# Kernel tuning notes

Measured on AMD Instinct MI355X. Metric: run time of the kernel, lower is better.

## Reference

```python
import jax, jax.numpy as jnp
import numpy as np

CLASS_TOKEN_INDEX = 1
MAX_PROMPTS = 25
MAX_TEXT_LEN = 3500
THRESHOLD = 0.5
B, S, D, E = 8, 4096, 768, 128
P = E * (E - 1) // 2  # 8128 candidate span pairs


def setup_inputs() -> dict:
    rng = np.random.default_rng(0)
    input_ids = rng.integers(5, 30000, size=(B, S)).astype(np.int64)
    words_mask = np.zeros((B, S), dtype=np.int64)
    attention_mask = np.zeros((B, S), dtype=np.int64)
    text_lengths = np.zeros((B, 1), dtype=np.int64)
    for b in range(B):
        ns = int(rng.integers(10, MAX_PROMPTS + 1))  # number of entity-type prompt tokens
        input_ids[b][input_ids[b] == CLASS_TOKEN_INDEX] = 5  # remove stray specials
        input_ids[b, :ns] = CLASS_TOKEN_INDEX
        L = int(rng.integers(3000, MAX_TEXT_LEN + 1))  # number of words in text
        words_mask[b, ns:ns + L] = np.arange(1, L + 1)
        attention_mask[b, :ns + L] = 1
        text_lengths[b, 0] = L
    key = jax.random.key(0)
    k1, k2, k3 = jax.random.split(key, 3)
    return {
        "token_embeds": jax.random.normal(k1, (B, S, D), dtype=jnp.float32),
        "adj": jax.random.uniform(k2, (B, E, E), dtype=jnp.float32),
        "span_rep": jax.random.normal(k3, (B, E, D), dtype=jnp.float32),
        "input_ids": jnp.asarray(input_ids),
        "attention_mask": jnp.asarray(attention_mask),
        "text_lengths": jnp.asarray(text_lengths),
        "words_mask": jnp.asarray(words_mask),
    }


def _extract_special(token_embeds, input_ids):
    # pack embeddings at positions where input_ids == class token, left-aligned
    special = input_ids == CLASS_TOKEN_INDEX                      # (B,S)
    num_special = special.sum(-1, keepdims=True)                  # (B,1)
    slot = jnp.cumsum(special, axis=-1) - 1                       # packed slot per special
    tgt = jnp.where(special, slot, MAX_PROMPTS)                   # dump pads into extra slot
    bidx = jnp.arange(B)[:, None]
    emb = jnp.zeros((B, MAX_PROMPTS + 1, D), token_embeds.dtype)
    emb = emb.at[bidx, tgt].add(token_embeds * special[..., None].astype(token_embeds.dtype))
    emb = emb[:, :MAX_PROMPTS]
    mask = (jnp.arange(MAX_PROMPTS)[None, :] < num_special).astype(jnp.int64)
    return emb, mask


def _extract_words(token_embeds, words_mask, text_lengths):
    # scatter token embeddings into word slots: words_embedding[b, words_mask[b,j]-1] = token_embeds[b,j]
    is_word = words_mask > 0
    tgt = jnp.where(is_word, words_mask - 1, MAX_TEXT_LEN)        # dump pads into extra slot
    bidx = jnp.arange(B)[:, None]
    we = jnp.zeros((B, MAX_TEXT_LEN + 1, D), token_embeds.dtype)
    we = we.at[bidx, tgt].add(token_embeds * is_word[..., None].astype(token_embeds.dtype))
    we = we[:, :MAX_TEXT_LEN]
    mask = jnp.arange(MAX_TEXT_LEN)[None, :] < text_lengths       # (B,MAX_TEXT_LEN) bool
    return we, mask


def _build_entity_pairs(adj, span_rep):
    rows, cols = jnp.triu_indices(E, k=1)                         # (P,), (P,)
    vals = adj[:, rows, cols]                                     # (B,P)
    sel = vals > THRESHOLD
    # stable left-packing: selected pairs first, preserving triu order (matches per-batch torch loop)
    order = jnp.argsort((~sel).astype(jnp.int32), axis=1, stable=True)
    pair_mask = jnp.take_along_axis(sel, order, axis=1)           # (B,P) bool
    r = rows[order]                                               # (B,P)
    c = cols[order]
    pair_idx = jnp.where(pair_mask[..., None], jnp.stack([r, c], axis=-1), -1)
    bidx = jnp.arange(B)[:, None]
    head_rep = span_rep[bidx, jnp.where(pair_mask, r, 0)]         # pads gather span 0 (clamp_min(0))
    tail_rep = span_rep[bidx, jnp.where(pair_mask, c, 0)]
    return pair_idx, pair_mask, head_rep, tail_rep


def reference(token_embeds, adj, span_rep, input_ids, attention_mask, text_lengths, words_mask):
    prompts_embedding, prompts_embedding_mask = _extract_special(token_embeds, input_ids)
    words_embedding, word_mask = _extract_words(token_embeds, words_mask, text_lengths)
    pair_idx, pair_mask, head_rep, tail_rep = _build_entity_pairs(adj, span_rep)
    return (prompts_embedding, prompts_embedding_mask, words_embedding, word_mask,
            pair_idx, pair_mask, head_rep, tail_rep)
```

## Files before the change

### kernel.cpp

```cpp
#include <hip/hip_runtime.h>

#define BB 8
#define SS 4096
#define DD 768
#define EE 128
#define PP 8128
#define MP 25
#define MT 3500
#define D4 192
#define NROWS_W  (BB*MT)
#define NROWS_P  (BB*PP)
#define NROWS_PR (BB*MP)
#define R_TOTAL  (NROWS_W + 2*NROWS_P + NROWS_PR)

typedef float f32x4 __attribute__((ext_vector_type(4)));

__global__ __launch_bounds__(1024) void k_prep(
    const int* __restrict__ ids, const float* __restrict__ adj,
    const int* __restrict__ wm, const int* __restrict__ tlen,
    float* __restrict__ out3,
    int* __restrict__ wordpos, int* __restrict__ pairrec,
    int* __restrict__ pos, int* __restrict__ nspec)
{
    int b = blockIdx.x;
    int t = threadIdx.x, wave = t >> 6, lane = t & 63;
    __shared__ int pos_s[MP];
    __shared__ int spos[16 * 32];
    __shared__ int wcnt[16];
    __shared__ int woff[17];
    __shared__ int wsum[16];

    if (t < MP) pos_s[t] = -1;

    {
        const int* row = ids + b * SS;
        int base = 0;
        for (int c = 0; c < 4; ++c) {
            int p = wave * 256 + c * 64 + lane;
            bool s = (row[p] == 1);
            unsigned long long m = __ballot(s);
            if (s) {
                int sl = base + __popcll(m & ((1ull << lane) - 1ull));
                if (sl < 32) spos[wave * 32 + sl] = p;
            }
            base += __popcll(m);
        }
        if (lane == 0) wcnt[wave] = base;
    }
    __syncthreads();
    if (t == 0) {
        int acc = 0;
        for (int w = 0; w < 16; ++w) { woff[w] = acc; acc += wcnt[w]; }
        woff[16] = acc;
    }
    __syncthreads();
    {
        int cnt = wcnt[wave]; if (cnt > 32) cnt = 32;
        if (lane < cnt) {
            int g = woff[wave] + lane;
            if (g < MP) pos_s[g] = spos[wave * 32 + lane];
        }
    }

    int L = tlen[b];
    for (int i = t; i < MT; i += 1024) {
        out3[b * MT + i] = (i < L) ? 1.0f : 0.0f;
        wordpos[b * MT + i] = -1;
    }
    __syncthreads();

    for (int i = t; i < SS; i += 1024) {
        int v = wm[b * SS + i];
        if (v > 0 && v <= MT) wordpos[b * MT + v - 1] = i;
    }
    if (t < MP) pos[b * MP + t] = pos_s[t];
    if (t == 0) nspec[b] = woff[16];

    int r8[8], c8[8]; bool s8[8]; int my = 0;
    for (int i = 0; i < 8; ++i) {
        int p = t * 8 + i;
        r8[i] = 0; c8[i] = 0; s8[i] = false;
        if (p < PP) {
            int lo = 0, hi = EE - 2;
            while (lo < hi) {
                int mid = (lo + hi + 1) >> 1;
                int st = mid * (2 * EE - 1 - mid) / 2;
                if (st <= p) lo = mid; else hi = mid - 1;
            }
            int r = lo;
            int st = r * (2 * EE - 1 - r) / 2;
            int c = r + 1 + (p - st);
            r8[i] = r; c8[i] = c;
            s8[i] = adj[((size_t)b * EE + r) * EE + c] > 0.5f;
            my += s8[i] ? 1 : 0;
        }
    }
    int inc = my;
    for (int off = 1; off < 64; off <<= 1) {
        int n = __shfl_up(inc, off);
        if (lane >= off) inc += n;
    }
    if (lane == 63) wsum[wave] = inc;
    __syncthreads();
    int wv_off = 0, K = 0;
    for (int w = 0; w < 16; ++w) {
        int s = wsum[w];
        if (w < wave) wv_off += s;
        K += s;
    }
    int selb = wv_off + inc - my;
    for (int i = 0; i < 8; ++i) {
        int p = t * 8 + i;
        if (p >= PP) break;
        int q;
        if (s8[i]) { q = selb; ++selb; }
        else       { q = K + (p - selb); }
        unsigned rec = s8[i] ? (0x80000000u | ((unsigned)r8[i] << 8) | (unsigned)c8[i]) : 0u;
        pairrec[(size_t)b * PP + q] = (int)rec;
    }
}

__global__ __launch_bounds__(256) void k_gather(
    const float* __restrict__ te, const float* __restrict__ sr,
    const int* __restrict__ wordpos, const int* __restrict__ pairrec,
    const int* __restrict__ pos, const int* __restrict__ nspec,
    float* __restrict__ out0, float* __restrict__ out1, float* __restrict__ out2,
    float* __restrict__ out4, float* __restrict__ out5,
    float* __restrict__ out6, float* __restrict__ out7)
{
    int gw = blockIdx.x * 4 + (threadIdx.x >> 6);
    int lane = threadIdx.x & 63;
    int nw = gridDim.x * 4;
    const f32x4* te4 = (const f32x4*)te;
    const f32x4* sr4 = (const f32x4*)sr;
    for (int row = gw; row < R_TOTAL; row += nw) {
        const f32x4* src4;
        f32x4* dst4;
        bool valid = true;
        bool stream_src = false;
        if (row < NROWS_W) {
            int b = row / MT;
            int s = wordpos[row];
            valid = (s >= 0);
            src4 = te4 + ((size_t)(b * SS + s)) * D4;
            dst4 = (f32x4*)out2 + (size_t)row * D4;
            stream_src = true;
        } else if (row < NROWS_W + 2 * NROWS_P) {
            int idx2 = row - NROWS_W;
            bool head = idx2 < NROWS_P;
            int idx = head ? idx2 : idx2 - NROWS_P;
            int b = idx / PP;
            unsigned rec = (unsigned)pairrec[idx];
            int r = (rec >> 8) & 0x7F;
            int c = rec & 0xFF;
            int s = head ? r : c;
            src4 = sr4 + ((size_t)(b * EE + s)) * D4;
            dst4 = (f32x4*)(head ? out6 : out7) + (size_t)idx * D4;
            if (head && lane == 0) {
                bool sel = rec != 0u;
                out4[(size_t)idx * 2 + 0] = sel ? (float)r : -1.0f;
                out4[(size_t)idx * 2 + 1] = sel ? (float)c : -1.0f;
                out5[idx] = sel ? 1.0f : 0.0f;
            }
        } else {
            int j2 = row - (NROWS_W + 2 * NROWS_P);
            int b = j2 / MP;
            int j = j2 - b * MP;
            int s = pos[j2];
            valid = (s >= 0);
            src4 = te4 + ((size_t)(b * SS + s)) * D4;
            dst4 = (f32x4*)out0 + (size_t)j2 * D4;
            stream_src = true;
            if (lane == 0) out1[j2] = (j < nspec[b]) ? 1.0f : 0.0f;
        }
        #pragma unroll
        for (int k = 0; k < 3; ++k) {
            f32x4 v = (f32x4)(0.0f);
            if (valid) {
                v = stream_src ? __builtin_nontemporal_load(&src4[lane + 64 * k])
                               : src4[lane + 64 * k];
            }
            dst4[lane + 64 * k] = v;
        }
    }
}

extern "C" void kernel_launch(void* const* d_in, const int* in_sizes, int n_in,
                              void* d_out, int out_size, void* d_ws, size_t ws_size,
                              hipStream_t stream) {
    const float* te   = (const float*)d_in[0];
    const float* adj  = (const float*)d_in[1];
    const float* sr   = (const float*)d_in[2];
    const int*   ids  = (const int*)d_in[3];
    const int*   tlen = (const int*)d_in[5];
    const int*   wm   = (const int*)d_in[6];
    float* out = (float*)d_out;

    size_t off0 = 0;
    size_t off1 = off0 + (size_t)BB * MP * DD;
    size_t off2 = off1 + (size_t)BB * MP;
    size_t off3 = off2 + (size_t)BB * MT * DD;
    size_t off4 = off3 + (size_t)BB * MT;
    size_t off5 = off4 + (size_t)BB * PP * 2;
    size_t off6 = off5 + (size_t)BB * PP;
    size_t off7 = off6 + (size_t)BB * PP * DD;

    int* wordpos = (int*)d_ws;
    int* pairrec = wordpos + BB * MT;
    int* pos     = pairrec + BB * PP;
    int* nspec   = pos + BB * MP;

    k_prep<<<BB, 1024, 0, stream>>>(ids, adj, wm, tlen, out + off3,
                                    wordpos, pairrec, pos, nspec);
    k_gather<<<2048, 256, 0, stream>>>(te, sr, wordpos, pairrec, pos, nspec,
                                       out + off0, out + off1, out + off2,
                                       out + off4, out + off5,
                                       out + off6, out + off7);
}
```

Before: 150.4 us.

## Split prep kernel into role blocks and prefetch next row index in gather

```diff
diff --git a/kernel.cpp b/kernel.cpp
--- a/kernel.cpp
+++ b/kernel.cpp
@@ -15,28 +15,29 @@
 
 typedef float f32x4 __attribute__((ext_vector_type(4)));
 
-__global__ __launch_bounds__(1024) void k_prep(
+__global__ __launch_bounds__(256) void k_prep(
     const int* __restrict__ ids, const float* __restrict__ adj,
     const int* __restrict__ wm, const int* __restrict__ tlen,
-    float* __restrict__ out3,
+    float* __restrict__ out1, float* __restrict__ out3,
+    float* __restrict__ out4, float* __restrict__ out5,
     int* __restrict__ wordpos, int* __restrict__ pairrec,
-    int* __restrict__ pos, int* __restrict__ nspec)
+    int* __restrict__ pos)
 {
-    int b = blockIdx.x;
+    int blk = blockIdx.x;
+    int role = blk >> 3, b = blk & 7;
     int t = threadIdx.x, wave = t >> 6, lane = t & 63;
-    __shared__ int pos_s[MP];
-    __shared__ int spos[16 * 32];
-    __shared__ int wcnt[16];
-    __shared__ int woff[17];
-    __shared__ int wsum[16];
-
-    if (t < MP) pos_s[t] = -1;
-
-    {
+
+    if (role == 0) {
+        __shared__ int pos_s[32];
+        __shared__ int spos[4 * 32];
+        __shared__ int wcnt[4];
+        __shared__ int woff[5];
+        if (t < 32) pos_s[t] = -1;
+        __syncthreads();
         const int* row = ids + b * SS;
         int base = 0;
-        for (int c = 0; c < 4; ++c) {
-            int p = wave * 256 + c * 64 + lane;
+        for (int c = 0; c < 16; ++c) {
+            int p = wave * 1024 + c * 64 + lane;
             bool s = (row[p] == 1);
             unsigned long long m = __ballot(s);
             if (s) {
@@ -46,86 +47,117 @@
             base += __popcll(m);
         }
         if (lane == 0) wcnt[wave] = base;
-    }
-    __syncthreads();
-    if (t == 0) {
-        int acc = 0;
-        for (int w = 0; w < 16; ++w) { woff[w] = acc; acc += wcnt[w]; }
-        woff[16] = acc;
-    }
-    __syncthreads();
-    {
-        int cnt = wcnt[wave]; if (cnt > 32) cnt = 32;
-        if (lane < cnt) {
-            int g = woff[wave] + lane;
-            if (g < MP) pos_s[g] = spos[wave * 32 + lane];
-        }
-    }
-
-    int L = tlen[b];
-    for (int i = t; i < MT; i += 1024) {
-        out3[b * MT + i] = (i < L) ? 1.0f : 0.0f;
-        wordpos[b * MT + i] = -1;
-    }
-    __syncthreads();
-
-    for (int i = t; i < SS; i += 1024) {
-        int v = wm[b * SS + i];
-        if (v > 0 && v <= MT) wordpos[b * MT + v - 1] = i;
-    }
-    if (t < MP) pos[b * MP + t] = pos_s[t];
-    if (t == 0) nspec[b] = woff[16];
-
-    int r8[8], c8[8]; bool s8[8]; int my = 0;
-    for (int i = 0; i < 8; ++i) {
-        int p = t * 8 + i;
-        r8[i] = 0; c8[i] = 0; s8[i] = false;
-        if (p < PP) {
+        __syncthreads();
+        if (t == 0) {
+            int acc = 0;
+            for (int w = 0; w < 4; ++w) { woff[w] = acc; acc += wcnt[w]; }
+            woff[4] = acc;
+        }
+        __syncthreads();
+        {
+            int cnt = wcnt[wave]; if (cnt > 32) cnt = 32;
+            if (lane < cnt) {
+                int g = woff[wave] + lane;
+                if (g < MP) pos_s[g] = spos[wave * 32 + lane];
+            }
+        }
+        __syncthreads();
+        if (t < MP) {
+            pos[b * MP + t] = pos_s[t];
+            out1[b * MP + t] = (t < woff[4]) ? 1.0f : 0.0f;
+        }
+    } else if (role == 1) {
+        int L = tlen[b];
+        for (int i = t; i < MT; i += 256) {
+            out3[b * MT + i] = (i < L) ? 1.0f : 0.0f;
+            wordpos[b * MT + i] = -1;
+        }
+        __syncthreads();
+        #pragma unroll 4
+        for (int i = t; i < SS; i += 256) {
+            int v = wm[b * SS + i];
+            if (v > 0 && v <= MT) wordpos[b * MT + v - 1] = i;
+        }
+    } else {
+        __shared__ int wsum[4];
+        int p0 = t * 32;
+        bool act = p0 < PP;
+        int r0 = 0, c0 = 0;
+        if (act) {
             int lo = 0, hi = EE - 2;
             while (lo < hi) {
                 int mid = (lo + hi + 1) >> 1;
                 int st = mid * (2 * EE - 1 - mid) / 2;
-                if (st <= p) lo = mid; else hi = mid - 1;
-            }
-            int r = lo;
-            int st = r * (2 * EE - 1 - r) / 2;
-            int c = r + 1 + (p - st);
-            r8[i] = r; c8[i] = c;
-            s8[i] = adj[((size_t)b * EE + r) * EE + c] > 0.5f;
-            my += s8[i] ? 1 : 0;
+                if (st <= p0) lo = mid; else hi = mid - 1;
+            }
+            r0 = lo;
+            c0 = r0 + 1 + (p0 - r0 * (2 * EE - 1 - r0) / 2);
+        }
+        unsigned selmask = 0;
+        int my = 0;
+        {
+            int rr = r0, cc = c0;
+            for (int i = 0; i < 32; ++i) {
+                if (act && p0 + i < PP) {
+                    bool s = adj[((size_t)b * EE + rr) * EE + cc] > 0.5f;
+                    selmask |= (unsigned)s << i;
+                    my += s ? 1 : 0;
+                    if (++cc == EE) { ++rr; cc = rr + 1; }
+                }
+            }
+        }
+        int inc = my;
+        for (int off = 1; off < 64; off <<= 1) {
+            int n = __shfl_up(inc, off);
+            if (lane >= off) inc += n;
+        }
+        if (lane == 63) wsum[wave] = inc;
+        __syncthreads();
+        int wv_off = 0, K = 0;
+        for (int w = 0; w < 4; ++w) {
+            int s = wsum[w];
+            if (w < wave) wv_off += s;
+            K += s;
+        }
+        int selb = wv_off + inc - my;
+        {
+            int rr = r0, cc = c0;
+            for (int i = 0; i < 32; ++i) {
+                int p = p0 + i;
+                if (act && p < PP) {
+                    bool s = (selmask >> i) & 1u;
+                    int q;
+                    if (s) { q = selb; ++selb; }
+                    else   { q = K + (p - selb); }
+                    size_t oq = (size_t)b * PP + q;
+                    pairrec[oq] = s ? (int)(0x80000000u | ((unsigned)rr << 8) | (unsigned)cc) : 0;
+                    out4[oq * 2 + 0] = s ? (float)rr : -1.0f;
+                    out4[oq * 2 + 1] = s ? (float)cc : -1.0f;
+                    out5[oq]         = s ? 1.0f : 0.0f;
+                    if (++cc == EE) { ++rr; cc = rr + 1; }
+                }
+            }
         }
     }
-    int inc = my;
-    for (int off = 1; off < 64; off <<= 1) {
-        int n = __shfl_up(inc, off);
-        if (lane >= off) inc += n;
+}
+
+__device__ __forceinline__ int row_index(const int* __restrict__ wordpos,
+                                         const int* __restrict__ pairrec,
+                                         const int* __restrict__ pos, int row) {
+    if (row < NROWS_W) return wordpos[row];
+    if (row < NROWS_W + 2 * NROWS_P) {
+        int idx2 = row - NROWS_W;
+        int idx = (idx2 < NROWS_P) ? idx2 : idx2 - NROWS_P;
+        return pairrec[idx];
     }
-    if (lane == 63) wsum[wave] = inc;
-    __syncthreads();
-    int wv_off = 0, K = 0;
-    for (int w = 0; w < 16; ++w) {
-        int s = wsum[w];
-        if (w < wave) wv_off += s;
-        K += s;
-    }
-    int selb = wv_off + inc - my;
-    for (int i = 0; i < 8; ++i) {
-        int p = t * 8 + i;
-        if (p >= PP) break;
-        int q;
-        if (s8[i]) { q = selb; ++selb; }
-        else       { q = K + (p - selb); }
-        unsigned rec = s8[i] ? (0x80000000u | ((unsigned)r8[i] << 8) | (unsigned)c8[i]) : 0u;
-        pairrec[(size_t)b * PP + q] = (int)rec;
-    }
+    return pos[row - (NROWS_W + 2 * NROWS_P)];
 }
 
 __global__ __launch_bounds__(256) void k_gather(
     const float* __restrict__ te, const float* __restrict__ sr,
     const int* __restrict__ wordpos, const int* __restrict__ pairrec,
-    const int* __restrict__ pos, const int* __restrict__ nspec,
-    float* __restrict__ out0, float* __restrict__ out1, float* __restrict__ out2,
-    float* __restrict__ out4, float* __restrict__ out5,
+    const int* __restrict__ pos,
+    float* __restrict__ out0, float* __restrict__ out2,
     float* __restrict__ out6, float* __restrict__ out7)
 {
     int gw = blockIdx.x * 4 + (threadIdx.x >> 6);
@@ -133,16 +165,22 @@
     int nw = gridDim.x * 4;
     const f32x4* te4 = (const f32x4*)te;
     const f32x4* sr4 = (const f32x4*)sr;
-    for (int row = gw; row < R_TOTAL; row += nw) {
+
+    int row = gw;
+    int iv = (row < R_TOTAL) ? row_index(wordpos, pairrec, pos, row) : 0;
+    for (; row < R_TOTAL; row += nw) {
+        int cur = iv;
+        int nrow = row + nw;
+        if (nrow < R_TOTAL) iv = row_index(wordpos, pairrec, pos, nrow);
+
         const f32x4* src4;
         f32x4* dst4;
         bool valid = true;
         bool stream_src = false;
         if (row < NROWS_W) {
             int b = row / MT;
-            int s = wordpos[row];
-            valid = (s >= 0);
-            src4 = te4 + ((size_t)(b * SS + s)) * D4;
+            valid = (cur >= 0);
+            src4 = te4 + ((size_t)(b * SS + (valid ? cur : 0))) * D4;
             dst4 = (f32x4*)out2 + (size_t)row * D4;
             stream_src = true;
         } else if (row < NROWS_W + 2 * NROWS_P) {
@@ -150,28 +188,17 @@
             bool head = idx2 < NROWS_P;
             int idx = head ? idx2 : idx2 - NROWS_P;
             int b = idx / PP;
-            unsigned rec = (unsigned)pairrec[idx];
-            int r = (rec >> 8) & 0x7F;
-            int c = rec & 0xFF;
-            int s = head ? r : c;
+            unsigned rec = (unsigned)cur;
+            int s = head ? ((rec >> 8) & 0x7F) : (rec & 0xFF);
             src4 = sr4 + ((size_t)(b * EE + s)) * D4;
             dst4 = (f32x4*)(head ? out6 : out7) + (size_t)idx * D4;
-            if (head && lane == 0) {
-                bool sel = rec != 0u;
-                out4[(size_t)idx * 2 + 0] = sel ? (float)r : -1.0f;
-                out4[(size_t)idx * 2 + 1] = sel ? (float)c : -1.0f;
-                out5[idx] = sel ? 1.0f : 0.0f;
-            }
         } else {
             int j2 = row - (NROWS_W + 2 * NROWS_P);
             int b = j2 / MP;
-            int j = j2 - b * MP;
-            int s = pos[j2];
-            valid = (s >= 0);
-            src4 = te4 + ((size_t)(b * SS + s)) * D4;
+            valid = (cur >= 0);
+            src4 = te4 + ((size_t)(b * SS + (valid ? cur : 0))) * D4;
             dst4 = (f32x4*)out0 + (size_t)j2 * D4;
             stream_src = true;
-            if (lane == 0) out1[j2] = (j < nspec[b]) ? 1.0f : 0.0f;
         }
         #pragma unroll
         for (int k = 0; k < 3; ++k) {
@@ -208,12 +235,11 @@
     int* wordpos = (int*)d_ws;
     int* pairrec = wordpos + BB * MT;
     int* pos     = pairrec + BB * PP;
-    int* nspec   = pos + BB * MP;
-
-    k_prep<<<BB, 1024, 0, stream>>>(ids, adj, wm, tlen, out + off3,
-                                    wordpos, pairrec, pos, nspec);
-    k_gather<<<2048, 256, 0, stream>>>(te, sr, wordpos, pairrec, pos, nspec,
-                                       out + off0, out + off1, out + off2,
-                                       out + off4, out + off5,
+
+    k_prep<<<24, 256, 0, stream>>>(ids, adj, wm, tlen,
+                                   out + off1, out + off3, out + off4, out + off5,
+                                   wordpos, pairrec, pos);
+    k_gather<<<2048, 256, 0, stream>>>(te, sr, wordpos, pairrec, pos,
+                                       out + off0, out + off2,
                                        out + off6, out + off7);
 }
```

Result: slower. 169.4 us (+12.7%).

## Split prep kernel into independent per-batch role blocks across 24 workgroups

Applied to the files above, without the earlier changes.

```diff
diff --git a/kernel.cpp b/kernel.cpp
--- a/kernel.cpp
+++ b/kernel.cpp
@@ -22,17 +22,17 @@
     int* __restrict__ wordpos, int* __restrict__ pairrec,
     int* __restrict__ pos, int* __restrict__ nspec)
 {
-    int b = blockIdx.x;
+    int blk = blockIdx.x;
+    int role = blk >> 3, b = blk & 7;
     int t = threadIdx.x, wave = t >> 6, lane = t & 63;
-    __shared__ int pos_s[MP];
-    __shared__ int spos[16 * 32];
-    __shared__ int wcnt[16];
-    __shared__ int woff[17];
-    __shared__ int wsum[16];
-
-    if (t < MP) pos_s[t] = -1;
-
-    {
+
+    if (role == 0) {
+        __shared__ int pos_s[MP];
+        __shared__ int spos[16 * 32];
+        __shared__ int wcnt[16];
+        __shared__ int woff[17];
+        if (t < MP) pos_s[t] = -1;
+        __syncthreads();
         const int* row = ids + b * SS;
         int base = 0;
         for (int c = 0; c < 4; ++c) {
@@ -46,77 +46,84 @@
             base += __popcll(m);
         }
         if (lane == 0) wcnt[wave] = base;
-    }
-    __syncthreads();
-    if (t == 0) {
-        int acc = 0;
-        for (int w = 0; w < 16; ++w) { woff[w] = acc; acc += wcnt[w]; }
-        woff[16] = acc;
-    }
-    __syncthreads();
-    {
-        int cnt = wcnt[wave]; if (cnt > 32) cnt = 32;
-        if (lane < cnt) {
-            int g = woff[wave] + lane;
-            if (g < MP) pos_s[g] = spos[wave * 32 + lane];
-        }
-    }
-
-    int L = tlen[b];
-    for (int i = t; i < MT; i += 1024) {
-        out3[b * MT + i] = (i < L) ? 1.0f : 0.0f;
-        wordpos[b * MT + i] = -1;
-    }
-    __syncthreads();
-
-    for (int i = t; i < SS; i += 1024) {
-        int v = wm[b * SS + i];
-        if (v > 0 && v <= MT) wordpos[b * MT + v - 1] = i;
-    }
-    if (t < MP) pos[b * MP + t] = pos_s[t];
-    if (t == 0) nspec[b] = woff[16];
-
-    int r8[8], c8[8]; bool s8[8]; int my = 0;
-    for (int i = 0; i < 8; ++i) {
-        int p = t * 8 + i;
-        r8[i] = 0; c8[i] = 0; s8[i] = false;
-        if (p < PP) {
-            int lo = 0, hi = EE - 2;
-            while (lo < hi) {
-                int mid = (lo + hi + 1) >> 1;
-                int st = mid * (2 * EE - 1 - mid) / 2;
-                if (st <= p) lo = mid; else hi = mid - 1;
-            }
-            int r = lo;
-            int st = r * (2 * EE - 1 - r) / 2;
-            int c = r + 1 + (p - st);
-            r8[i] = r; c8[i] = c;
-            s8[i] = adj[((size_t)b * EE + r) * EE + c] > 0.5f;
-            my += s8[i] ? 1 : 0;
-        }
-    }
-    int inc = my;
-    for (int off = 1; off < 64; off <<= 1) {
-        int n = __shfl_up(inc, off);
-        if (lane >= off) inc += n;
-    }
-    if (lane == 63) wsum[wave] = inc;
-    __syncthreads();
-    int wv_off = 0, K = 0;
-    for (int w = 0; w < 16; ++w) {
-        int s = wsum[w];
-        if (w < wave) wv_off += s;
-        K += s;
-    }
-    int selb = wv_off + inc - my;
-    for (int i = 0; i < 8; ++i) {
-        int p = t * 8 + i;
-        if (p >= PP) break;
-        int q;
-        if (s8[i]) { q = selb; ++selb; }
-        else       { q = K + (p - selb); }
-        unsigned rec = s8[i] ? (0x80000000u | ((unsigned)r8[i] << 8) | (unsigned)c8[i]) : 0u;
-        pairrec[(size_t)b * PP + q] = (int)rec;
+        __syncthreads();
+        if (t == 0) {
+            int acc = 0;
+            for (int w = 0; w < 16; ++w) { woff[w] = acc; acc += wcnt[w]; }
+            woff[16] = acc;
+        }
+        __syncthreads();
+        {
+            int cnt = wcnt[wave]; if (cnt > 32) cnt = 32;
+            if (lane < cnt) {
+                int g = woff[wave] + lane;
+                if (g < MP) pos_s[g] = spos[wave * 32 + lane];
+            }
+        }
+        __syncthreads();
+        if (t < MP) pos[b * MP + t] = pos_s[t];
+        if (t == 0) nspec[b] = woff[16];
+    } else if (role == 1) {
+        int L = tlen[b];
+        for (int i = t; i < MT; i += 1024) {
+            out3[b * MT + i] = (i < L) ? 1.0f : 0.0f;
+            wordpos[b * MT + i] = -1;
+        }
+        __syncthreads();
+        for (int i = t; i < SS; i += 1024) {
+            int v = wm[b * SS + i];
+            if (v > 0 && v <= MT) wordpos[b * MT + v - 1] = i;
+        }
+    } else {
+        __shared__ unsigned long long wmask[8][16];
+        __shared__ int wsum[8][16];
+        for (int ch = 0; ch < 8; ++ch) {
+            int p = ch * 1024 + t;
+            bool s = false;
+            if (p < PP) {
+                int lo = 0, hi = EE - 2;
+                while (lo < hi) {
+                    int mid = (lo + hi + 1) >> 1;
+                    int st = mid * (2 * EE - 1 - mid) / 2;
+                    if (st <= p) lo = mid; else hi = mid - 1;
+                }
+                int r = lo;
+                int c = r + 1 + (p - r * (2 * EE - 1 - r) / 2);
+                s = adj[((size_t)b * EE + r) * EE + c] > 0.5f;
+            }
+            unsigned long long m = __ballot(s);
+            if (lane == 0) { wmask[ch][wave] = m; wsum[ch][wave] = __popcll(m); }
+        }
+        __syncthreads();
+        int K = 0;
+        for (int ch = 0; ch < 8; ++ch)
+            for (int w = 0; w < 16; ++w) K += wsum[ch][w];
+        int cbase = 0;
+        for (int ch = 0; ch < 8; ++ch) {
+            int p = ch * 1024 + t;
+            if (p < PP) {
+                unsigned long long m = wmask[ch][wave];
+                bool s = (m >> lane) & 1ull;
+                int woffw = 0;
+                for (int w = 0; w < wave; ++w) woffw += wsum[ch][w];
+                int rank = cbase + woffw + __popcll(m & ((1ull << lane) - 1ull));
+                int q = s ? rank : (K + (p - rank));
+                int rec = 0;
+                if (s) {
+                    int lo = 0, hi = EE - 2;
+                    while (lo < hi) {
+                        int mid = (lo + hi + 1) >> 1;
+                        int st = mid * (2 * EE - 1 - mid) / 2;
+                        if (st <= p) lo = mid; else hi = mid - 1;
+                    }
+                    int r = lo;
+                    int c = r + 1 + (p - r * (2 * EE - 1 - r) / 2);
+                    rec = (int)(0x80000000u | ((unsigned)r << 8) | (unsigned)c);
+                }
+                pairrec[(size_t)b * PP + q] = rec;
+            }
+            for (int w = 0; w < 16; ++w) cbase += wsum[ch][w];
+        }
     }
 }
 
@@ -142,7 +149,7 @@
             int b = row / MT;
             int s = wordpos[row];
             valid = (s >= 0);
-            src4 = te4 + ((size_t)(b * SS + s)) * D4;
+            src4 = te4 + ((size_t)(b * SS + (valid ? s : 0))) * D4;
             dst4 = (f32x4*)out2 + (size_t)row * D4;
             stream_src = true;
         } else if (row < NROWS_W + 2 * NROWS_P) {
@@ -168,7 +175,7 @@
             int j = j2 - b * MP;
             int s = pos[j2];
             valid = (s >= 0);
-            src4 = te4 + ((size_t)(b * SS + s)) * D4;
+            src4 = te4 + ((size_t)(b * SS + (valid ? s : 0))) * D4;
             dst4 = (f32x4*)out0 + (size_t)j2 * D4;
             stream_src = true;
             if (lane == 0) out1[j2] = (j < nspec[b]) ? 1.0f : 0.0f;
@@ -210,7 +217,7 @@
     int* pos     = pairrec + BB * PP;
     int* nspec   = pos + BB * MP;
 
-    k_prep<<<BB, 1024, 0, stream>>>(ids, adj, wm, tlen, out + off3,
+    k_prep<<<24, 1024, 0, stream>>>(ids, adj, wm, tlen, out + off3,
                                     wordpos, pairrec, pos, nspec);
     k_gather<<<2048, 256, 0, stream>>>(te, sr, wordpos, pairrec, pos, nspec,
                                        out + off0, out + off1, out + off2,
```

Result: slower. 156.8 us (+4.2%).
